# Performance work log

Hardware: AMD Instinct MI355X
Metric: run time of the kernel (lower is better)

Reference implementation:

```python
import jax, jax.numpy as jnp
import numpy as np

B, H, W = 32, 128, 128
NA = 9            # number of anchors
STRIDE = 16.0
CLS_THRESH = 0.95
MAX_IOU = 0.1
NUM_PROP = 10
NEG = -1e9        # sentinel for suppressed / below-threshold scores


def setup_inputs() -> dict:
    key = jax.random.key(0)
    inputs = jax.random.normal(key, (B, H, W, NA * 4 + NA + 1), dtype=jnp.float32)
    anchors = jnp.array([[0.5, 32.0], [1.0, 32.0], [2.0, 32.0],
                         [0.5, 64.0], [1.0, 64.0], [2.0, 64.0],
                         [0.5, 128.0], [1.0, 128.0], [2.0, 128.0]], dtype=jnp.float32)
    return {"inputs": inputs, "anchors": anchors}


def _decode(inputs, anchors):
    b, h, w, c = inputs.shape
    cls = inputs[..., -1]
    # zero out 1-pixel border (the tf.pad'ed cancel matrix)
    border = jnp.zeros((h, w), inputs.dtype).at[1:-1, 1:-1].set(1.0)
    cls = cls * border
    a_reg = inputs[..., -10:-1]           # [B,H,W,9]
    bbox_reg = inputs[..., :-10]          # [B,H,W,36]
    a_idx = jnp.argmax(a_reg, axis=-1)    # [B,H,W] best anchor per position
    # gather the 4 deltas of the chosen anchor: channels a_idx*4 .. a_idx*4+3
    gidx = a_idx[..., None] * 4 + jnp.arange(4)
    deltas = jnp.take_along_axis(bbox_reg, gidx, axis=-1)          # [B,H,W,4]
    anc = anchors[a_idx].astype(jnp.float32)                       # [B,H,W,2]
    # anchor box: center x from column, center y from row, height=anc[:,1], width=anc[:,1]/anc[:,0]
    ax = (jnp.arange(w, dtype=jnp.float32)[None, :] + 0.5) * STRIDE  # [1,W]
    ay = (jnp.arange(h, dtype=jnp.float32)[:, None] + 0.5) * STRIDE  # [H,1]
    a0 = jnp.broadcast_to(ax, (h, w))[None]                          # [1,H,W]
    a1 = jnp.broadcast_to(ay, (h, w))[None]
    a2 = anc[..., 1]
    a3 = anc[..., 1] / anc[..., 0]
    b0 = deltas[..., 0] * a2 + a0
    b1 = deltas[..., 1] * a3 + a1
    b2 = jnp.exp(deltas[..., 2]) * a2
    b3 = jnp.exp(deltas[..., 3]) * a3
    bboxes = jnp.stack([b0, b1, b2, b3], axis=-1)                    # [B,H,W,4]
    coords = jnp.stack([b1 - b3 / 2, b0 - b2 / 2,
                        b1 + b3 / 2, b0 + b2 / 2], axis=-1)          # [y1,x1,y2,x2]
    scores = jnp.where(cls > CLS_THRESH, cls, NEG)                   # mask below-threshold
    n = h * w
    return (bboxes.reshape(b, n, 4), coords.reshape(b, n, 4), scores.reshape(b, n))


def _nms_one(boxes, coords, scores):
    # greedy NMS, equivalent to tf.image.non_max_suppression over the valid candidates
    n = scores.shape[0]
    area = jnp.maximum(coords[:, 2] - coords[:, 0], 0.0) * jnp.maximum(coords[:, 3] - coords[:, 1], 0.0)
    idx_range = jnp.arange(n)

    def body(i, state):
        sc, out = state
        j = jnp.argmax(sc)
        ok = sc[j] > NEG / 2
        sel = coords[j]
        iy1 = jnp.maximum(coords[:, 0], sel[0])
        ix1 = jnp.maximum(coords[:, 1], sel[1])
        iy2 = jnp.minimum(coords[:, 2], sel[2])
        ix2 = jnp.minimum(coords[:, 3], sel[3])
        inter = jnp.maximum(iy2 - iy1, 0.0) * jnp.maximum(ix2 - ix1, 0.0)
        area_s = jnp.maximum(sel[2] - sel[0], 0.0) * jnp.maximum(sel[3] - sel[1], 0.0)
        iou = inter / (area + area_s - inter + 1e-10)
        suppress = (iou > MAX_IOU) | (idx_range == j)
        sc = jnp.where(ok & suppress, NEG, sc)
        out = out.at[i].set(jnp.where(ok, boxes[j], jnp.zeros(4, boxes.dtype)))
        return sc, out

    out0 = jnp.zeros((NUM_PROP, 4), boxes.dtype)
    _, out = jax.lax.fori_loop(0, NUM_PROP, body, (scores, out0))
    return out


def _forward(inputs, anchors):
    bboxes, coords, scores = _decode(inputs, anchors)
    return jax.vmap(_nms_one)(bboxes, coords, scores)   # [B, NUM_PROP, 4]


def reference(inputs, anchors):
    return _forward(inputs, anchors)
```

## Files before the change

kernel.cpp:

```cpp
#include <hip/hip_runtime.h>
#include <math.h>

#define BB 32
#define HH 128
#define WW 128
#define NA 9
#define CCH 46
#define NPIX (HH*WW)
#define STRIDE_F 16.0f
#define CLS_T 0.95f
#define MAX_IOU_F 0.1f
#define NUM_PROP 10
#define NEGV -1000000000.0f

#define TILE_PIX 256
#define TILE_FLOATS (TILE_PIX * CCH)
#define TILE_VEC (TILE_FLOATS / 4)

#define NTILE (BB * NPIX / TILE_PIX)
#define NWAVES (NTILE * 4)
#define WSLOT 64

#define NMS_T 512
#define MAXPER 10
#define MMAX (MAXPER * NMS_T)

#define GLL16(gp, lp)                                                          \
  __builtin_amdgcn_global_load_lds(                                            \
      (__attribute__((address_space(1))) void*)(gp),                           \
      (__attribute__((address_space(3))) void*)(lp), 16, 0, 0)

__global__ __launch_bounds__(256, 3) void decode_kernel(
    const float* __restrict__ in, const float* __restrict__ anchors,
    int* __restrict__ wcnt, float* __restrict__ sc_comp,
    float4* __restrict__ co_comp)
{
  __shared__ float s_in[TILE_FLOATS];

  int tid = threadIdx.x;
  int tile = blockIdx.x;
  int g0 = tile * TILE_PIX;

  const float4* srcv = (const float4*)(in + (size_t)g0 * CCH);
  float4* dstv = (float4*)s_in;
#pragma unroll
  for (int i = 0; i < 12; ++i) {
    int k = tid + i * 256;
    if (k < TILE_VEC)
      GLL16(srcv + k, dstv + k);
  }
  __syncthreads();

  int g = g0 + tid;
  int p = g & (NPIX - 1);
  int h = p >> 7;
  int w = p & (WW - 1);
  const float* px = s_in + tid * CCH;

  float cls = px[45];
  bool interior = (h >= 1) && (h <= HH - 2) && (w >= 1) && (w <= WW - 2);
  bool cand = interior && (cls > CLS_T);

  unsigned long long mask = __ballot(cand);
  int lane = tid & 63;
  int waveid = tile * 4 + (tid >> 6);
  int total = __popcll(mask);
  if (lane == 0) wcnt[waveid] = total;

  if (!cand) return;

  int ai = 0; float av = px[36];
#pragma unroll
  for (int c = 1; c < NA; ++c) { float v = px[36 + c]; if (v > av) { av = v; ai = c; } }

  float d0 = px[ai * 4 + 0], d1 = px[ai * 4 + 1];
  float d2 = px[ai * 4 + 2], d3 = px[ai * 4 + 3];
  float ratio = anchors[ai * 2 + 0], sz = anchors[ai * 2 + 1];
  float a2 = sz, a3 = sz / ratio;
  float ax = ((float)w + 0.5f) * STRIDE_F;
  float ay = ((float)h + 0.5f) * STRIDE_F;
  float b0 = d0 * a2 + ax;
  float b1 = d1 * a3 + ay;
  float b2 = expf(d2) * a2;
  float b3 = expf(d3) * a3;
  float4 co = make_float4(b1 - 0.5f * b3, b0 - 0.5f * b2,
                          b1 + 0.5f * b3, b0 + 0.5f * b2);

  int prefix = __popcll(mask & ((1ull << lane) - 1ull));
  int slot = waveid * WSLOT + prefix;
  sc_comp[slot] = cls;
  co_comp[slot] = co;
}

__global__ __launch_bounds__(NMS_T, 1) void nms_kernel(
    const int* __restrict__ wcnt, const float* __restrict__ sc_comp,
    const float4* __restrict__ co_comp, float* __restrict__ out)
{
  __shared__ float  s_sc[MMAX];
  __shared__ float4 s_co[MMAX];
  __shared__ int    s_tmp[256];
  __shared__ float  s_rv[8];
  __shared__ int    s_rk[8];
  __shared__ float  s_jv;
  __shared__ int    s_jk;

  int b = blockIdx.x, tid = threadIdx.x;

  int c = 0;
  if (tid < 256) { c = wcnt[b * 256 + tid]; s_tmp[tid] = c; }
  __syncthreads();
  for (int d = 1; d < 256; d <<= 1) {
    int v = 0;
    if (tid < 256) { v = s_tmp[tid]; if (tid >= d) v += s_tmp[tid - d]; }
    __syncthreads();
    if (tid < 256) s_tmp[tid] = v;
    __syncthreads();
  }
  if (tid < 256) {
    int excl = s_tmp[tid] - c;
    const float*  sp = sc_comp + (size_t)(b * 256 + tid) * WSLOT;
    const float4* cp = co_comp + (size_t)(b * 256 + tid) * WSLOT;
    for (int i = 0; i < c; ++i) {
      int d = excl + i;
      if (d < MMAX) { s_sc[d] = sp[i]; s_co[d] = cp[i]; }
    }
  }
  __syncthreads();
  int M = s_tmp[255]; if (M > MMAX) M = MMAX;

  float  sc[MAXPER];
  float4 co[MAXPER];
  float  ar[MAXPER];
#pragma unroll
  for (int r = 0; r < MAXPER; ++r) {
    int k = r * NMS_T + tid;
    if (k < M) {
      sc[r] = s_sc[k];
      co[r] = s_co[k];
      ar[r] = fmaxf(co[r].z - co[r].x, 0.f) * fmaxf(co[r].w - co[r].y, 0.f);
    } else {
      sc[r] = NEGV; co[r] = make_float4(0.f, 0.f, 0.f, 0.f); ar[r] = 0.f;
    }
  }

  for (int it = 0; it < NUM_PROP; ++it) {
    float bv = -INFINITY; int bk = 0x7fffffff;
#pragma unroll
    for (int r = 0; r < MAXPER; ++r) {
      if (sc[r] > bv) { bv = sc[r]; bk = r * NMS_T + tid; }
    }
    for (int off = 32; off > 0; off >>= 1) {
      float ov = __shfl_down(bv, off);
      int   ok_ = __shfl_down(bk, off);
      if (ov > bv || (ov == bv && ok_ < bk)) { bv = ov; bk = ok_; }
    }
    int wv = tid >> 6;
    if ((tid & 63) == 0) { s_rv[wv] = bv; s_rk[wv] = bk; }
    __syncthreads();
    if (tid == 0) {
      float fv = s_rv[0]; int fk = s_rk[0];
#pragma unroll
      for (int q = 1; q < 8; ++q) {
        if (s_rv[q] > fv || (s_rv[q] == fv && s_rk[q] < fk)) { fv = s_rv[q]; fk = s_rk[q]; }
      }
      s_jv = fv; s_jk = fk;
    }
    __syncthreads();
    float jv = s_jv;
    bool okq = jv > (NEGV * 0.5f);

    if (okq) {
      int jk = s_jk;
      float4 selc = s_co[jk];
      float sy1 = selc.x, sx1 = selc.y, sy2 = selc.z, sx2 = selc.w;
      float sarea = fmaxf(sy2 - sy1, 0.f) * fmaxf(sx2 - sx1, 0.f);
#pragma unroll
      for (int r = 0; r < MAXPER; ++r) {
        float4 cc = co[r];
        float iy1 = fmaxf(cc.x, sy1);
        float ix1 = fmaxf(cc.y, sx1);
        float iy2 = fminf(cc.z, sy2);
        float ix2 = fminf(cc.w, sx2);
        float inter = fmaxf(iy2 - iy1, 0.f) * fmaxf(ix2 - ix1, 0.f);
        float iou = inter / (ar[r] + sarea - inter + 1e-10f);
        if (iou > MAX_IOU_F || (r * NMS_T + tid) == jk) sc[r] = NEGV;
      }
      if (tid == 0) {
        float* o = out + (size_t)(b * NUM_PROP + it) * 4;
        o[0] = 0.5f * (sx1 + sx2);
        o[1] = 0.5f * (sy1 + sy2);
        o[2] = sx2 - sx1;
        o[3] = sy2 - sy1;
      }
    } else if (tid == 0) {
      float* o = out + (size_t)(b * NUM_PROP + it) * 4;
      o[0] = 0.f; o[1] = 0.f; o[2] = 0.f; o[3] = 0.f;
    }
    __syncthreads();
  }
}

extern "C" void kernel_launch(void* const* d_in, const int* in_sizes, int n_in,
                              void* d_out, int out_size, void* d_ws, size_t ws_size,
                              hipStream_t stream) {
  const float* in      = (const float*)d_in[0];
  const float* anchors = (const float*)d_in[1];
  float* out = (float*)d_out;

  char* ws = (char*)d_ws;
  int*    wcnt    = (int*)ws;
  float4* co_comp = (float4*)(ws + (size_t)NWAVES * 4);
  float*  sc_comp = (float*)(ws + (size_t)NWAVES * 4 + (size_t)NWAVES * WSLOT * 16);

  decode_kernel<<<NTILE, 256, 0, stream>>>(in, anchors, wcnt, sc_comp, co_comp);
  nms_kernel<<<BB, NMS_T, 0, stream>>>(wcnt, sc_comp, co_comp, out);
}
```

Before: 171.6 us.

## Streamline NMS kernel: wave-shuffle scan, direct global gather, single-barrier argmax

Replaces the 256-wide shared-memory Hillis-Steele scan with a wave-level shuffle scan plus cross-wave totals, and removes the staging of candidates into shared memory by having each thread binary-search the prefix array and load its candidates straight from the compacted global buffers. The per-iteration argmax now carries the box coordinates through the shuffles and uses double-buffered per-wave results, so every thread does the final 8-way reduction itself and one barrier per iteration is dropped. The loop exits early once no valid candidate remains, zero-filling the remaining outputs. In exchange there are more shuffles per reduction step and scattered global reads with a binary search per element.

```diff
diff --git a/kernel.cpp b/kernel.cpp
--- a/kernel.cpp
+++ b/kernel.cpp
@@ -96,37 +96,31 @@
     const int* __restrict__ wcnt, const float* __restrict__ sc_comp,
     const float4* __restrict__ co_comp, float* __restrict__ out)
 {
-  __shared__ float  s_sc[MMAX];
-  __shared__ float4 s_co[MMAX];
-  __shared__ int    s_tmp[256];
-  __shared__ float  s_rv[8];
-  __shared__ int    s_rk[8];
-  __shared__ float  s_jv;
-  __shared__ int    s_jk;
+  __shared__ int    s_pref[256];
+  __shared__ int    s_wtot[4];
+  __shared__ float  s_rv[2][8];
+  __shared__ int    s_rk[2][8];
+  __shared__ float4 s_rc[2][8];
 
   int b = blockIdx.x, tid = threadIdx.x;
-
-  int c = 0;
-  if (tid < 256) { c = wcnt[b * 256 + tid]; s_tmp[tid] = c; }
+  int lane = tid & 63, wv = tid >> 6;
+
+  int c = (tid < 256) ? wcnt[b * 256 + tid] : 0;
+  int v = c;
+#pragma unroll
+  for (int off = 1; off < 64; off <<= 1) {
+    int u = __shfl_up(v, off);
+    if (lane >= off) v += u;
+  }
+  if (wv < 4 && lane == 63) s_wtot[wv] = v;
   __syncthreads();
-  for (int d = 1; d < 256; d <<= 1) {
-    int v = 0;
-    if (tid < 256) { v = s_tmp[tid]; if (tid >= d) v += s_tmp[tid - d]; }
-    __syncthreads();
-    if (tid < 256) s_tmp[tid] = v;
-    __syncthreads();
-  }
-  if (tid < 256) {
-    int excl = s_tmp[tid] - c;
-    const float*  sp = sc_comp + (size_t)(b * 256 + tid) * WSLOT;
-    const float4* cp = co_comp + (size_t)(b * 256 + tid) * WSLOT;
-    for (int i = 0; i < c; ++i) {
-      int d = excl + i;
-      if (d < MMAX) { s_sc[d] = sp[i]; s_co[d] = cp[i]; }
-    }
-  }
+  int add = 0;
+#pragma unroll
+  for (int q = 0; q < 3; ++q) if (q < wv) add += s_wtot[q];
+  if (tid < 256) s_pref[tid] = v + add;
   __syncthreads();
-  int M = s_tmp[255]; if (M > MMAX) M = MMAX;
+  int M = s_pref[255];
+  if (M > MMAX) M = MMAX;
 
   float  sc[MAXPER];
   float4 co[MAXPER];
@@ -135,44 +129,55 @@
   for (int r = 0; r < MAXPER; ++r) {
     int k = r * NMS_T + tid;
     if (k < M) {
-      sc[r] = s_sc[k];
-      co[r] = s_co[k];
+      int lo = 0, hi = 255;
+#pragma unroll
+      for (int s = 0; s < 8; ++s) {
+        int mid = (lo + hi) >> 1;
+        if (s_pref[mid] > k) hi = mid; else lo = mid + 1;
+      }
+      int excl = (lo > 0) ? s_pref[lo - 1] : 0;
+      size_t base = (size_t)(b * 256 + lo) * WSLOT + (k - excl);
+      sc[r] = sc_comp[base];
+      co[r] = co_comp[base];
       ar[r] = fmaxf(co[r].z - co[r].x, 0.f) * fmaxf(co[r].w - co[r].y, 0.f);
     } else {
       sc[r] = NEGV; co[r] = make_float4(0.f, 0.f, 0.f, 0.f); ar[r] = 0.f;
     }
   }
 
+  int buf = 0;
   for (int it = 0; it < NUM_PROP; ++it) {
     float bv = -INFINITY; int bk = 0x7fffffff;
+    float4 bc = make_float4(0.f, 0.f, 0.f, 0.f);
 #pragma unroll
     for (int r = 0; r < MAXPER; ++r) {
-      if (sc[r] > bv) { bv = sc[r]; bk = r * NMS_T + tid; }
-    }
+      if (sc[r] > bv) { bv = sc[r]; bk = r * NMS_T + tid; bc = co[r]; }
+    }
+#pragma unroll
     for (int off = 32; off > 0; off >>= 1) {
-      float ov = __shfl_down(bv, off);
+      float ov  = __shfl_down(bv, off);
       int   ok_ = __shfl_down(bk, off);
-      if (ov > bv || (ov == bv && ok_ < bk)) { bv = ov; bk = ok_; }
-    }
-    int wv = tid >> 6;
-    if ((tid & 63) == 0) { s_rv[wv] = bv; s_rk[wv] = bk; }
+      float ox  = __shfl_down(bc.x, off);
+      float oy  = __shfl_down(bc.y, off);
+      float oz  = __shfl_down(bc.z, off);
+      float ow  = __shfl_down(bc.w, off);
+      if (ov > bv || (ov == bv && ok_ < bk)) {
+        bv = ov; bk = ok_; bc = make_float4(ox, oy, oz, ow);
+      }
+    }
+    if (lane == 0) { s_rv[buf][wv] = bv; s_rk[buf][wv] = bk; s_rc[buf][wv] = bc; }
     __syncthreads();
-    if (tid == 0) {
-      float fv = s_rv[0]; int fk = s_rk[0];
-#pragma unroll
-      for (int q = 1; q < 8; ++q) {
-        if (s_rv[q] > fv || (s_rv[q] == fv && s_rk[q] < fk)) { fv = s_rv[q]; fk = s_rk[q]; }
-      }
-      s_jv = fv; s_jk = fk;
-    }
-    __syncthreads();
-    float jv = s_jv;
+    float jv = s_rv[buf][0]; int jk = s_rk[buf][0]; float4 jc = s_rc[buf][0];
+#pragma unroll
+    for (int q = 1; q < 8; ++q) {
+      float qv = s_rv[buf][q]; int qk = s_rk[buf][q];
+      if (qv > jv || (qv == jv && qk < jk)) { jv = qv; jk = qk; jc = s_rc[buf][q]; }
+    }
+    buf ^= 1;
+
     bool okq = jv > (NEGV * 0.5f);
-
     if (okq) {
-      int jk = s_jk;
-      float4 selc = s_co[jk];
-      float sy1 = selc.x, sx1 = selc.y, sy2 = selc.z, sx2 = selc.w;
+      float sy1 = jc.x, sx1 = jc.y, sy2 = jc.z, sx2 = jc.w;
       float sarea = fmaxf(sy2 - sy1, 0.f) * fmaxf(sx2 - sx1, 0.f);
 #pragma unroll
       for (int r = 0; r < MAXPER; ++r) {
@@ -192,11 +197,15 @@
         o[2] = sx2 - sx1;
         o[3] = sy2 - sy1;
       }
-    } else if (tid == 0) {
-      float* o = out + (size_t)(b * NUM_PROP + it) * 4;
-      o[0] = 0.f; o[1] = 0.f; o[2] = 0.f; o[3] = 0.f;
-    }
-    __syncthreads();
+    } else {
+      if (tid == 0) {
+        for (int it2 = it; it2 < NUM_PROP; ++it2) {
+          float* o = out + (size_t)(b * NUM_PROP + it2) * 4;
+          o[0] = 0.f; o[1] = 0.f; o[2] = 0.f; o[3] = 0.f;
+        }
+      }
+      break;
+    }
   }
 }
 
```

New measurement: 171.9 us. No clear change (+0.2%).
